# Kernel optimization log

Measured on AMD Instinct MI355X. Metric: run time of the kernel, lower is better.

## Reference

```python
import jax, jax.numpy as jnp
import numpy as np

N_NODES = 500_000
N_EDGES = 32_000_000
D_COEF = 1.0  # 'd' init arg, constant


def setup_inputs() -> dict:
    key = jax.random.key(0)
    k1, k2, k3 = jax.random.split(key, 3)
    theta = jax.random.normal(k1, (N_NODES, 1), dtype=jnp.float32)
    src = jax.random.randint(k2, (N_EDGES,), 0, N_NODES, dtype=jnp.int32)
    dst = jax.random.randint(k3, (N_EDGES,), 0, N_NODES, dtype=jnp.int32)
    logc = jnp.asarray(np.log(1.5), dtype=jnp.float32)  # continuousTimeVicsek2D.logc
    u0 = jnp.asarray(0.3, dtype=jnp.float32)
    return {"theta": theta, "logc": logc, "u0": u0, "src": src, "dst": dst}


def reference(theta, logc, u0, src, dst):
    # calc_message: dtheta = theta[src] - theta[dst]; m = exp(logc)*sin(d*dtheta)
    dtheta = theta[src] - theta[dst]              # [E,1] edge gather
    msg = jnp.exp(logc) * jnp.sin(dtheta * D_COEF)  # [E,1]
    # aggregate_message: mean over each node's incoming mailbox (segment mean by dst)
    n = theta.shape[0]
    w_sum = jax.ops.segment_sum(msg, dst, num_segments=n)          # [N,1]
    cnt = jax.ops.segment_sum(jnp.ones((dst.shape[0], 1), msg.dtype), dst, num_segments=n)
    w = w_sum / jnp.maximum(cnt, 1.0)             # [N,1] torque (0 if no in-edges)
    # polarity2velocity: v = u0 * [cos(theta), sin(theta)]
    v = u0 * jnp.concatenate([jnp.cos(theta), jnp.sin(theta)], axis=-1)  # [N,2]
    # return torque and velocity concatenated: [N,3] = [w | v]
    return jnp.concatenate([w, v], axis=-1)
```

## Files before the change

kernel.cpp:

```cpp
#include <hip/hip_runtime.h>


#define NB 123
#define BSHIFT 12
#define NODES_PER_B 4096
#define CAPB 272000u
#define TPB 256
#define EPT 16
#define EPI (TPB * EPT)
#define K_SLICES 8
#define TPB_R 512
#define Q_MASK 0xFFFFFu
#define DL_SHIFT 20

typedef int iv4 __attribute__((ext_vector_type(4)));

__device__ __forceinline__ float theta_l2(const float* p) {
    return __hip_atomic_load(p, __ATOMIC_RELAXED, __HIP_MEMORY_SCOPE_AGENT);
}

__global__ __launch_bounds__(TPB) void scatter_kernel(
    const float* __restrict__ theta,
    const int* __restrict__ src,
    const int* __restrict__ dst,
    unsigned int* __restrict__ recs,
    unsigned int* __restrict__ cursors,
    int n_edges, int n_iters)
{
    __shared__ unsigned int hist[NB];
    __shared__ unsigned int rankc[NB];
    __shared__ unsigned int offs[NB];
    __shared__ unsigned int gbase[NB];
    __shared__ unsigned int wsum0;
    __shared__ unsigned int sbuf[EPI];
    __shared__ unsigned char sbkt[EPI];

    const int tid = threadIdx.x;

    for (int iter = blockIdx.x; iter < n_iters; iter += gridDim.x) {
        const int base = iter * EPI + tid * EPT;

        for (int j = tid; j < NB; j += TPB) { hist[j] = 0; rankc[j] = 0; }
        __syncthreads();

        unsigned int myrec[EPT];
        int myb[EPT];

        if (base + EPT <= n_edges) {
            iv4 s4[4], d4[4];
            #pragma unroll
            for (int q = 0; q < 4; ++q) {
                s4[q] = __builtin_nontemporal_load(((const iv4*)(src + base)) + q);
                d4[q] = __builtin_nontemporal_load(((const iv4*)(dst + base)) + q);
            }
            const int* sp = (const int*)s4;
            const int* dp = (const int*)d4;
            float tg[EPT];
            #pragma unroll
            for (int j = 0; j < EPT; ++j) tg[j] = theta_l2(theta + sp[j]);
            #pragma unroll
            for (int j = 0; j < EPT; ++j) {
                int b = dp[j] >> BSHIFT;
                myb[j] = b;
                atomicAdd(&hist[b], 1u);
            }
            #pragma unroll
            for (int j = 0; j < EPT; ++j) {
                float tc = fminf(fmaxf(tg[j], -8.0f), 8.0f);
                unsigned int q = (unsigned int)fmaf(tc, 65536.0f, 524288.5f);
                if (q > Q_MASK) q = Q_MASK;
                myrec[j] = (((unsigned int)(dp[j] & (NODES_PER_B - 1))) << DL_SHIFT) | q;
            }
        } else {
            #pragma unroll
            for (int j = 0; j < EPT; ++j) {
                int e = base + j;
                if (e < n_edges) {
                    int dn = dst[e];
                    float tc = fminf(fmaxf(theta_l2(theta + src[e]), -8.0f), 8.0f);
                    unsigned int q = (unsigned int)fmaf(tc, 65536.0f, 524288.5f);
                    if (q > Q_MASK) q = Q_MASK;
                    myrec[j] = (((unsigned int)(dn & (NODES_PER_B - 1))) << DL_SHIFT) | q;
                    int b = dn >> BSHIFT;
                    myb[j] = b;
                    atomicAdd(&hist[b], 1u);
                } else {
                    myb[j] = -1;
                }
            }
        }
        __syncthreads();

        unsigned int h = 0, x = 0;
        if (tid < 128) {
            h = (tid < NB) ? hist[tid] : 0u;
            x = h;
            #pragma unroll
            for (int dlt = 1; dlt < 64; dlt <<= 1) {
                unsigned int y = __shfl_up(x, dlt, 64);
                if ((tid & 63) >= dlt) x += y;
            }
            if (tid == 63) wsum0 = x;
        }
        __syncthreads();
        if (tid < 128) {
            if (tid >= 64) x += wsum0;
            if (tid < NB) {
                offs[tid] = x - h;
                gbase[tid] = h ? atomicAdd(&cursors[tid], h) : 0u;
            }
        }
        __syncthreads();

        #pragma unroll
        for (int j = 0; j < EPT; ++j) {
            int b = myb[j];
            if (b >= 0) {
                unsigned int r = atomicAdd(&rankc[b], 1u);
                unsigned int slot = offs[b] + r;
                sbuf[slot] = myrec[j];
                sbkt[slot] = (unsigned char)b;
            }
        }
        __syncthreads();

        unsigned int total = offs[NB - 1] + hist[NB - 1];
        for (unsigned int slot = tid; slot < total; slot += TPB) {
            unsigned int b = sbkt[slot];
            unsigned int gpos = gbase[b] + (slot - offs[b]);
            if (gpos < CAPB) recs[(size_t)b * CAPB + gpos] = sbuf[slot];
        }
        __syncthreads();
    }
}

__device__ __forceinline__ void proc_rec(unsigned int ru, unsigned long long* acc)
{
    float t = fmaf((float)(ru & Q_MASK), 1.0f / 65536.0f, -8.0f);
    float s, co;
    __sincosf(t, &s, &co);
    unsigned int ps = (unsigned int)fmaf(s, 8192.0f, 16384.5f);
    unsigned int pc = (unsigned int)fmaf(co, 8192.0f, 16384.5f);
    atomicAdd(&acc[ru >> DL_SHIFT],
              ((unsigned long long)ps << 37) | ((unsigned long long)pc << 10) | 1ull);
}

__global__ __launch_bounds__(TPB_R, 8) void reduce_kernel(
    const unsigned int* __restrict__ recs,
    const unsigned int* __restrict__ cursors,
    unsigned long long* __restrict__ acc_g)
{
    __shared__ unsigned long long acc[NODES_PER_B];
    const int tid = threadIdx.x;
    const int b = blockIdx.x >> 3;
    const int k = blockIdx.x & 7;

    for (int j = tid; j < NODES_PER_B; j += TPB_R) acc[j] = 0ull;
    __syncthreads();

    unsigned int cnt = cursors[b];
    if (cnt > CAPB) cnt = CAPB;
    unsigned int slice = (((cnt + K_SLICES - 1) / K_SLICES) + 15u) & ~15u;
    unsigned int lo = (unsigned int)k * slice;
    if (lo > cnt) lo = cnt;
    unsigned int hi = lo + slice; if (hi > cnt) hi = cnt;

    const unsigned int* bp = recs + (size_t)b * CAPB;

    const unsigned int chunk = TPB_R * 4u;
    unsigned int nfull = (hi > lo) ? (hi - lo) / chunk : 0u;
    unsigned int vend = lo + nfull * chunk;

    for (unsigned int b2 = lo; b2 < vend; b2 += chunk) {
        uint4 r = *(const uint4*)(bp + b2 + (unsigned int)tid * 4u);
        proc_rec(r.x, acc);
        proc_rec(r.y, acc);
        proc_rec(r.z, acc);
        proc_rec(r.w, acc);
    }
    for (unsigned int j = vend + tid; j < hi; j += TPB_R) proc_rec(bp[j], acc);
    __syncthreads();

    unsigned long long* ag = acc_g + (size_t)b * NODES_PER_B;
    for (int j = tid; j < NODES_PER_B; j += TPB_R) {
        unsigned long long v = acc[j];
        if (v) atomicAdd(&ag[j], v);
    }
}

__global__ __launch_bounds__(TPB) void node_kernel(
    const float* __restrict__ theta,
    const float* __restrict__ logc,
    const float* __restrict__ u0p,
    const unsigned long long* __restrict__ acc_g,
    float* __restrict__ out,
    int n_nodes)
{
    int i = blockIdx.x * TPB + threadIdx.x;
    if (i >= n_nodes) return;

    unsigned long long a = acc_g[i];
    int cnt = (int)(a & 1023ull);
    int pcS = (int)((a >> 10) & 0x7FFFFFFull);
    int psS = (int)(a >> 37);
    float sinS = (float)(psS - cnt * 16384) * (1.0f / 8192.0f);
    float cosS = (float)(pcS - cnt * 16384) * (1.0f / 8192.0f);

    float t = theta[i];
    float sd, cd;
    __sincosf(t, &sd, &cd);
    float c = __expf(logc[0]);
    float w = c * (cd * sinS - sd * cosS) / fmaxf((float)cnt, 1.0f);
    float u0 = u0p[0];
    out[3 * i + 0] = w;
    out[3 * i + 1] = u0 * cd;
    out[3 * i + 2] = u0 * sd;
}

__global__ __launch_bounds__(256) void edge_kernel_fb(
    const float* __restrict__ theta, const float* __restrict__ logc,
    const int* __restrict__ src, const int* __restrict__ dst,
    unsigned long long* __restrict__ acc, int n_edges)
{
    const float c = __expf(logc[0]);
    int base = (blockIdx.x * 256 + threadIdx.x) * 4;
    if (base + 3 < n_edges) {
        int4 s4 = *(const int4*)(src + base);
        int4 d4 = *(const int4*)(dst + base);
        float m0 = c * __sinf(theta[s4.x] - theta[d4.x]);
        float m1 = c * __sinf(theta[s4.y] - theta[d4.y]);
        float m2 = c * __sinf(theta[s4.z] - theta[d4.z]);
        float m3 = c * __sinf(theta[s4.w] - theta[d4.w]);
        atomicAdd(&acc[d4.x], ((unsigned long long)((m0 + 2.0f) * 1073741824.0f) << 24) | 1ull);
        atomicAdd(&acc[d4.y], ((unsigned long long)((m1 + 2.0f) * 1073741824.0f) << 24) | 1ull);
        atomicAdd(&acc[d4.z], ((unsigned long long)((m2 + 2.0f) * 1073741824.0f) << 24) | 1ull);
        atomicAdd(&acc[d4.w], ((unsigned long long)((m3 + 2.0f) * 1073741824.0f) << 24) | 1ull);
    } else {
        for (int e = base; e < n_edges; ++e) {
            int s = src[e], d = dst[e];
            float m = c * __sinf(theta[s] - theta[d]);
            atomicAdd(&acc[d], ((unsigned long long)((m + 2.0f) * 1073741824.0f) << 24) | 1ull);
        }
    }
}

__global__ __launch_bounds__(256) void node_kernel_fb(
    const float* __restrict__ theta, const float* __restrict__ u0p,
    const unsigned long long* __restrict__ acc, float* __restrict__ out, int n_nodes)
{
    int i = blockIdx.x * 256 + threadIdx.x;
    if (i >= n_nodes) return;
    unsigned long long p = acc[i];
    long long cnt = (long long)(p & 0xFFFFFFull);
    long long net = (long long)(p >> 24) - (cnt << 31);
    float sum = (float)((double)net * (1.0 / 1073741824.0));
    float w = sum / fmaxf((float)cnt, 1.0f);
    float t = theta[i]; float u0 = u0p[0];
    out[3 * i + 0] = w;
    out[3 * i + 1] = u0 * __cosf(t);
    out[3 * i + 2] = u0 * __sinf(t);
}

extern "C" void kernel_launch(void* const* d_in, const int* in_sizes, int n_in,
                              void* d_out, int out_size, void* d_ws, size_t ws_size,
                              hipStream_t stream) {
    const float* theta = (const float*)d_in[0];
    const float* logc  = (const float*)d_in[1];
    const float* u0    = (const float*)d_in[2];
    const int*   src   = (const int*)d_in[3];
    const int*   dst   = (const int*)d_in[4];
    float* out = (float*)d_out;

    int n_nodes = in_sizes[0];
    int n_edges = in_sizes[3];

    size_t recs_bytes  = (size_t)NB * CAPB * sizeof(unsigned int);
    size_t cursors_off = (recs_bytes + 255) & ~(size_t)255;
    size_t acc_off     = cursors_off + 512;
    size_t acc_bytes   = (size_t)NB * NODES_PER_B * sizeof(unsigned long long);
    size_t need = acc_off + acc_bytes;

    bool fast = (ws_size >= need) && (n_nodes <= NB * NODES_PER_B);

    if (fast) {
        unsigned int* recs          = (unsigned int*)d_ws;
        unsigned int* cursors       = (unsigned int*)((char*)d_ws + cursors_off);
        unsigned long long* acc_g   = (unsigned long long*)((char*)d_ws + acc_off);

        (void)hipMemsetAsync(cursors, 0, 512 + acc_bytes, stream);

        int n_iters = (n_edges + EPI - 1) / EPI;
        scatter_kernel<<<n_iters, TPB, 0, stream>>>(theta, src, dst, recs,
                                                    cursors, n_edges, n_iters);

        reduce_kernel<<<NB * K_SLICES, TPB_R, 0, stream>>>(recs, cursors, acc_g);

        int nblocks = (n_nodes + TPB - 1) / TPB;
        node_kernel<<<nblocks, TPB, 0, stream>>>(theta, logc, u0, acc_g, out, n_nodes);
    } else {
        unsigned long long* acc = (unsigned long long*)d_ws;
        (void)hipMemsetAsync(d_ws, 0, (size_t)n_nodes * sizeof(unsigned long long), stream);
        int eblocks = (n_edges + 1023) / 1024;
        edge_kernel_fb<<<eblocks, 256, 0, stream>>>(theta, logc, src, dst, acc, n_edges);
        int nblocks = (n_nodes + 255) / 256;
        node_kernel_fb<<<nblocks, 256, 0, stream>>>(theta, u0, acc, out, n_nodes);
    }
}
```

Before: 482.1 us.

## Replace bucketed scatter/reduce with direct global 64-bit packed atomics per edge

Drops the two-pass bucket scatter into a record workspace followed by per-bucket LDS reduction. Each edge now computes sin/cos of its source theta and adds a packed 64-bit value straight into a global per-node accumulator. This removes the record write and re-read and the LDS bucketing passes, but sends 32M random 64-bit atomics to global memory/L2. It also removes the fallback path and the workspace-size check.

```diff
diff --git a/kernel.cpp b/kernel.cpp
--- a/kernel.cpp
+++ b/kernel.cpp
@@ -1,190 +1,55 @@
 #include <hip/hip_runtime.h>
 
 
-#define NB 123
-#define BSHIFT 12
-#define NODES_PER_B 4096
-#define CAPB 272000u
 #define TPB 256
 #define EPT 16
 #define EPI (TPB * EPT)
-#define K_SLICES 8
-#define TPB_R 512
-#define Q_MASK 0xFFFFFu
-#define DL_SHIFT 20
 
 typedef int iv4 __attribute__((ext_vector_type(4)));
 
-__device__ __forceinline__ float theta_l2(const float* p) {
-    return __hip_atomic_load(p, __ATOMIC_RELAXED, __HIP_MEMORY_SCOPE_AGENT);
-}
-
-__global__ __launch_bounds__(TPB) void scatter_kernel(
+__global__ __launch_bounds__(TPB) void edge_lin_kernel(
     const float* __restrict__ theta,
     const int* __restrict__ src,
     const int* __restrict__ dst,
-    unsigned int* __restrict__ recs,
-    unsigned int* __restrict__ cursors,
-    int n_edges, int n_iters)
+    unsigned long long* __restrict__ acc,
+    int n_edges)
 {
-    __shared__ unsigned int hist[NB];
-    __shared__ unsigned int rankc[NB];
-    __shared__ unsigned int offs[NB];
-    __shared__ unsigned int gbase[NB];
-    __shared__ unsigned int wsum0;
-    __shared__ unsigned int sbuf[EPI];
-    __shared__ unsigned char sbkt[EPI];
+    const int base = (blockIdx.x * TPB + threadIdx.x) * EPT;
 
-    const int tid = threadIdx.x;
+    if (base + EPT <= n_edges) {
+        iv4 s4[4], d4[4];
+        #pragma unroll
+        for (int q = 0; q < 4; ++q) {
+            s4[q] = __builtin_nontemporal_load(((const iv4*)(src + base)) + q);
+            d4[q] = __builtin_nontemporal_load(((const iv4*)(dst + base)) + q);
+        }
+        const int* sp = (const int*)s4;
+        const int* dp = (const int*)d4;
 
-    for (int iter = blockIdx.x; iter < n_iters; iter += gridDim.x) {
-        const int base = iter * EPI + tid * EPT;
-
-        for (int j = tid; j < NB; j += TPB) { hist[j] = 0; rankc[j] = 0; }
-        __syncthreads();
-
-        unsigned int myrec[EPT];
-        int myb[EPT];
-
-        if (base + EPT <= n_edges) {
-            iv4 s4[4], d4[4];
-            #pragma unroll
-            for (int q = 0; q < 4; ++q) {
-                s4[q] = __builtin_nontemporal_load(((const iv4*)(src + base)) + q);
-                d4[q] = __builtin_nontemporal_load(((const iv4*)(dst + base)) + q);
-            }
-            const int* sp = (const int*)s4;
-            const int* dp = (const int*)d4;
-            float tg[EPT];
-            #pragma unroll
-            for (int j = 0; j < EPT; ++j) tg[j] = theta_l2(theta + sp[j]);
-            #pragma unroll
-            for (int j = 0; j < EPT; ++j) {
-                int b = dp[j] >> BSHIFT;
-                myb[j] = b;
-                atomicAdd(&hist[b], 1u);
-            }
-            #pragma unroll
-            for (int j = 0; j < EPT; ++j) {
-                float tc = fminf(fmaxf(tg[j], -8.0f), 8.0f);
-                unsigned int q = (unsigned int)fmaf(tc, 65536.0f, 524288.5f);
-                if (q > Q_MASK) q = Q_MASK;
-                myrec[j] = (((unsigned int)(dp[j] & (NODES_PER_B - 1))) << DL_SHIFT) | q;
-            }
-        } else {
-            #pragma unroll
-            for (int j = 0; j < EPT; ++j) {
-                int e = base + j;
-                if (e < n_edges) {
-                    int dn = dst[e];
-                    float tc = fminf(fmaxf(theta_l2(theta + src[e]), -8.0f), 8.0f);
-                    unsigned int q = (unsigned int)fmaf(tc, 65536.0f, 524288.5f);
-                    if (q > Q_MASK) q = Q_MASK;
-                    myrec[j] = (((unsigned int)(dn & (NODES_PER_B - 1))) << DL_SHIFT) | q;
-                    int b = dn >> BSHIFT;
-                    myb[j] = b;
-                    atomicAdd(&hist[b], 1u);
-                } else {
-                    myb[j] = -1;
-                }
-            }
-        }
-        __syncthreads();
-
-        unsigned int h = 0, x = 0;
-        if (tid < 128) {
-            h = (tid < NB) ? hist[tid] : 0u;
-            x = h;
-            #pragma unroll
-            for (int dlt = 1; dlt < 64; dlt <<= 1) {
-                unsigned int y = __shfl_up(x, dlt, 64);
-                if ((tid & 63) >= dlt) x += y;
-            }
-            if (tid == 63) wsum0 = x;
-        }
-        __syncthreads();
-        if (tid < 128) {
-            if (tid >= 64) x += wsum0;
-            if (tid < NB) {
-                offs[tid] = x - h;
-                gbase[tid] = h ? atomicAdd(&cursors[tid], h) : 0u;
-            }
-        }
-        __syncthreads();
+        float tg[EPT];
+        #pragma unroll
+        for (int j = 0; j < EPT; ++j) tg[j] = theta[sp[j]];
 
         #pragma unroll
         for (int j = 0; j < EPT; ++j) {
-            int b = myb[j];
-            if (b >= 0) {
-                unsigned int r = atomicAdd(&rankc[b], 1u);
-                unsigned int slot = offs[b] + r;
-                sbuf[slot] = myrec[j];
-                sbkt[slot] = (unsigned char)b;
-            }
+            float s, co;
+            __sincosf(tg[j], &s, &co);
+            unsigned int ps = (unsigned int)fmaf(s,  8192.0f, 16384.5f);
+            unsigned int pc = (unsigned int)fmaf(co, 8192.0f, 16384.5f);
+            atomicAdd(&acc[dp[j]],
+                      ((unsigned long long)ps << 37) |
+                      ((unsigned long long)pc << 10) | 1ull);
         }
-        __syncthreads();
-
-        unsigned int total = offs[NB - 1] + hist[NB - 1];
-        for (unsigned int slot = tid; slot < total; slot += TPB) {
-            unsigned int b = sbkt[slot];
-            unsigned int gpos = gbase[b] + (slot - offs[b]);
-            if (gpos < CAPB) recs[(size_t)b * CAPB + gpos] = sbuf[slot];
+    } else {
+        for (int e = base; e < n_edges; ++e) {
+            float s, co;
+            __sincosf(theta[src[e]], &s, &co);
+            unsigned int ps = (unsigned int)fmaf(s,  8192.0f, 16384.5f);
+            unsigned int pc = (unsigned int)fmaf(co, 8192.0f, 16384.5f);
+            atomicAdd(&acc[dst[e]],
+                      ((unsigned long long)ps << 37) |
+                      ((unsigned long long)pc << 10) | 1ull);
         }
-        __syncthreads();
-    }
-}
-
-__device__ __forceinline__ void proc_rec(unsigned int ru, unsigned long long* acc)
-{
-    float t = fmaf((float)(ru & Q_MASK), 1.0f / 65536.0f, -8.0f);
-    float s, co;
-    __sincosf(t, &s, &co);
-    unsigned int ps = (unsigned int)fmaf(s, 8192.0f, 16384.5f);
-    unsigned int pc = (unsigned int)fmaf(co, 8192.0f, 16384.5f);
-    atomicAdd(&acc[ru >> DL_SHIFT],
-              ((unsigned long long)ps << 37) | ((unsigned long long)pc << 10) | 1ull);
-}
-
-__global__ __launch_bounds__(TPB_R, 8) void reduce_kernel(
-    const unsigned int* __restrict__ recs,
-    const unsigned int* __restrict__ cursors,
-    unsigned long long* __restrict__ acc_g)
-{
-    __shared__ unsigned long long acc[NODES_PER_B];
-    const int tid = threadIdx.x;
-    const int b = blockIdx.x >> 3;
-    const int k = blockIdx.x & 7;
-
-    for (int j = tid; j < NODES_PER_B; j += TPB_R) acc[j] = 0ull;
-    __syncthreads();
-
-    unsigned int cnt = cursors[b];
-    if (cnt > CAPB) cnt = CAPB;
-    unsigned int slice = (((cnt + K_SLICES - 1) / K_SLICES) + 15u) & ~15u;
-    unsigned int lo = (unsigned int)k * slice;
-    if (lo > cnt) lo = cnt;
-    unsigned int hi = lo + slice; if (hi > cnt) hi = cnt;
-
-    const unsigned int* bp = recs + (size_t)b * CAPB;
-
-    const unsigned int chunk = TPB_R * 4u;
-    unsigned int nfull = (hi > lo) ? (hi - lo) / chunk : 0u;
-    unsigned int vend = lo + nfull * chunk;
-
-    for (unsigned int b2 = lo; b2 < vend; b2 += chunk) {
-        uint4 r = *(const uint4*)(bp + b2 + (unsigned int)tid * 4u);
-        proc_rec(r.x, acc);
-        proc_rec(r.y, acc);
-        proc_rec(r.z, acc);
-        proc_rec(r.w, acc);
-    }
-    for (unsigned int j = vend + tid; j < hi; j += TPB_R) proc_rec(bp[j], acc);
-    __syncthreads();
-
-    unsigned long long* ag = acc_g + (size_t)b * NODES_PER_B;
-    for (int j = tid; j < NODES_PER_B; j += TPB_R) {
-        unsigned long long v = acc[j];
-        if (v) atomicAdd(&ag[j], v);
     }
 }
 
@@ -192,14 +57,14 @@
     const float* __restrict__ theta,
     const float* __restrict__ logc,
     const float* __restrict__ u0p,
-    const unsigned long long* __restrict__ acc_g,
+    const unsigned long long* __restrict__ acc,
     float* __restrict__ out,
     int n_nodes)
 {
     int i = blockIdx.x * TPB + threadIdx.x;
     if (i >= n_nodes) return;
 
-    unsigned long long a = acc_g[i];
+    unsigned long long a = acc[i];
     int cnt = (int)(a & 1023ull);
     int pcS = (int)((a >> 10) & 0x7FFFFFFull);
     int psS = (int)(a >> 37);
@@ -220,45 +85,9 @@
 __global__ __launch_bounds__(256) void edge_kernel_fb(
     const float* __restrict__ theta, const float* __restrict__ logc,
     const int* __restrict__ src, const int* __restrict__ dst,
-    unsigned long long* __restrict__ acc, int n_edges)
+    float* __restrict__ out, int n_edges)
 {
-    const float c = __expf(logc[0]);
-    int base = (blockIdx.x * 256 + threadIdx.x) * 4;
-    if (base + 3 < n_edges) {
-        int4 s4 = *(const int4*)(src + base);
-        int4 d4 = *(const int4*)(dst + base);
-        float m0 = c * __sinf(theta[s4.x] - theta[d4.x]);
-        float m1 = c * __sinf(theta[s4.y] - theta[d4.y]);
-        float m2 = c * __sinf(theta[s4.z] - theta[d4.z]);
-        float m3 = c * __sinf(theta[s4.w] - theta[d4.w]);
-        atomicAdd(&acc[d4.x], ((unsigned long long)((m0 + 2.0f) * 1073741824.0f) << 24) | 1ull);
-        atomicAdd(&acc[d4.y], ((unsigned long long)((m1 + 2.0f) * 1073741824.0f) << 24) | 1ull);
-        atomicAdd(&acc[d4.z], ((unsigned long long)((m2 + 2.0f) * 1073741824.0f) << 24) | 1ull);
-        atomicAdd(&acc[d4.w], ((unsigned long long)((m3 + 2.0f) * 1073741824.0f) << 24) | 1ull);
-    } else {
-        for (int e = base; e < n_edges; ++e) {
-            int s = src[e], d = dst[e];
-            float m = c * __sinf(theta[s] - theta[d]);
-            atomicAdd(&acc[d], ((unsigned long long)((m + 2.0f) * 1073741824.0f) << 24) | 1ull);
-        }
-    }
-}
-
-__global__ __launch_bounds__(256) void node_kernel_fb(
-    const float* __restrict__ theta, const float* __restrict__ u0p,
-    const unsigned long long* __restrict__ acc, float* __restrict__ out, int n_nodes)
-{
-    int i = blockIdx.x * 256 + threadIdx.x;
-    if (i >= n_nodes) return;
-    unsigned long long p = acc[i];
-    long long cnt = (long long)(p & 0xFFFFFFull);
-    long long net = (long long)(p >> 24) - (cnt << 31);
-    float sum = (float)((double)net * (1.0 / 1073741824.0));
-    float w = sum / fmaxf((float)cnt, 1.0f);
-    float t = theta[i]; float u0 = u0p[0];
-    out[3 * i + 0] = w;
-    out[3 * i + 1] = u0 * __cosf(t);
-    out[3 * i + 2] = u0 * __sinf(t);
+    (void)theta; (void)logc; (void)src; (void)dst; (void)out; (void)n_edges;
 }
 
 extern "C" void kernel_launch(void* const* d_in, const int* in_sizes, int n_in,
@@ -274,35 +103,14 @@
     int n_nodes = in_sizes[0];
     int n_edges = in_sizes[3];
 
-    size_t recs_bytes  = (size_t)NB * CAPB * sizeof(unsigned int);
-    size_t cursors_off = (recs_bytes + 255) & ~(size_t)255;
-    size_t acc_off     = cursors_off + 512;
-    size_t acc_bytes   = (size_t)NB * NODES_PER_B * sizeof(unsigned long long);
-    size_t need = acc_off + acc_bytes;
+    unsigned long long* acc = (unsigned long long*)d_ws;
 
-    bool fast = (ws_size >= need) && (n_nodes <= NB * NODES_PER_B);
+    (void)hipMemsetAsync(acc, 0, (size_t)n_nodes * sizeof(unsigned long long),
+                         stream);
 
-    if (fast) {
-        unsigned int* recs          = (unsigned int*)d_ws;
-        unsigned int* cursors       = (unsigned int*)((char*)d_ws + cursors_off);
-        unsigned long long* acc_g   = (unsigned long long*)((char*)d_ws + acc_off);
+    int eblocks = (n_edges + EPI - 1) / EPI;
+    edge_lin_kernel<<<eblocks, TPB, 0, stream>>>(theta, src, dst, acc, n_edges);
 
-        (void)hipMemsetAsync(cursors, 0, 512 + acc_bytes, stream);
-
-        int n_iters = (n_edges + EPI - 1) / EPI;
-        scatter_kernel<<<n_iters, TPB, 0, stream>>>(theta, src, dst, recs,
-                                                    cursors, n_edges, n_iters);
-
-        reduce_kernel<<<NB * K_SLICES, TPB_R, 0, stream>>>(recs, cursors, acc_g);
-
-        int nblocks = (n_nodes + TPB - 1) / TPB;
-        node_kernel<<<nblocks, TPB, 0, stream>>>(theta, logc, u0, acc_g, out, n_nodes);
-    } else {
-        unsigned long long* acc = (unsigned long long*)d_ws;
-        (void)hipMemsetAsync(d_ws, 0, (size_t)n_nodes * sizeof(unsigned long long), stream);
-        int eblocks = (n_edges + 1023) / 1024;
-        edge_kernel_fb<<<eblocks, 256, 0, stream>>>(theta, logc, src, dst, acc, n_edges);
-        int nblocks = (n_nodes + 255) / 256;
-        node_kernel_fb<<<nblocks, 256, 0, stream>>>(theta, u0, acc, out, n_nodes);
-    }
+    int nblocks = (n_nodes + TPB - 1) / TPB;
+    node_kernel<<<nblocks, TPB, 0, stream>>>(theta, logc, u0, acc, out, n_nodes);
 }
```

Result: slower. 1.589 ms (+229.6%).

## Write per-slice partials instead of global atomics, reuse histogram ranks, nontemporal stores

Applied to the files above, without the earlier changes.

The reduce kernel now writes each slice's shared-memory accumulator into its own partials buffer instead of atomically adding into a global accumulator. The node kernel sums the 8 slices per node, which removes the large memset and the global atomics. The scatter kernel takes each edge's rank from the histogram atomic's return value, dropping the second rank-counter atomic pass. Theta gathers become plain loads, and record stores and loads become nontemporal. The cost is more partials memory (8x) and 8 reads per node in the final kernel.

```diff
diff --git a/kernel.cpp b/kernel.cpp
--- a/kernel.cpp
+++ b/kernel.cpp
@@ -14,10 +14,7 @@
 #define DL_SHIFT 20
 
 typedef int iv4 __attribute__((ext_vector_type(4)));
-
-__device__ __forceinline__ float theta_l2(const float* p) {
-    return __hip_atomic_load(p, __ATOMIC_RELAXED, __HIP_MEMORY_SCOPE_AGENT);
-}
+typedef unsigned int uv4 __attribute__((ext_vector_type(4)));
 
 __global__ __launch_bounds__(TPB) void scatter_kernel(
     const float* __restrict__ theta,
@@ -28,7 +25,6 @@
     int n_edges, int n_iters)
 {
     __shared__ unsigned int hist[NB];
-    __shared__ unsigned int rankc[NB];
     __shared__ unsigned int offs[NB];
     __shared__ unsigned int gbase[NB];
     __shared__ unsigned int wsum0;
@@ -40,11 +36,11 @@
     for (int iter = blockIdx.x; iter < n_iters; iter += gridDim.x) {
         const int base = iter * EPI + tid * EPT;
 
-        for (int j = tid; j < NB; j += TPB) { hist[j] = 0; rankc[j] = 0; }
+        for (int j = tid; j < NB; j += TPB) hist[j] = 0;
         __syncthreads();
 
         unsigned int myrec[EPT];
-        int myb[EPT];
+        unsigned int mybr[EPT];
 
         if (base + EPT <= n_edges) {
             iv4 s4[4], d4[4];
@@ -57,12 +53,12 @@
             const int* dp = (const int*)d4;
             float tg[EPT];
             #pragma unroll
-            for (int j = 0; j < EPT; ++j) tg[j] = theta_l2(theta + sp[j]);
+            for (int j = 0; j < EPT; ++j) tg[j] = theta[sp[j]];
             #pragma unroll
             for (int j = 0; j < EPT; ++j) {
                 int b = dp[j] >> BSHIFT;
-                myb[j] = b;
-                atomicAdd(&hist[b], 1u);
+                unsigned int r = atomicAdd(&hist[b], 1u);
+                mybr[j] = ((unsigned int)b << 12) | r;
             }
             #pragma unroll
             for (int j = 0; j < EPT; ++j) {
@@ -77,15 +73,15 @@
                 int e = base + j;
                 if (e < n_edges) {
                     int dn = dst[e];
-                    float tc = fminf(fmaxf(theta_l2(theta + src[e]), -8.0f), 8.0f);
+                    float tc = fminf(fmaxf(theta[src[e]], -8.0f), 8.0f);
                     unsigned int q = (unsigned int)fmaf(tc, 65536.0f, 524288.5f);
                     if (q > Q_MASK) q = Q_MASK;
                     myrec[j] = (((unsigned int)(dn & (NODES_PER_B - 1))) << DL_SHIFT) | q;
                     int b = dn >> BSHIFT;
-                    myb[j] = b;
-                    atomicAdd(&hist[b], 1u);
+                    unsigned int r = atomicAdd(&hist[b], 1u);
+                    mybr[j] = ((unsigned int)b << 12) | r;
                 } else {
-                    myb[j] = -1;
+                    mybr[j] = 0xFFFFFFFFu;
                 }
             }
         }
@@ -114,10 +110,10 @@
 
         #pragma unroll
         for (int j = 0; j < EPT; ++j) {
-            int b = myb[j];
-            if (b >= 0) {
-                unsigned int r = atomicAdd(&rankc[b], 1u);
-                unsigned int slot = offs[b] + r;
+            unsigned int br = mybr[j];
+            if (br != 0xFFFFFFFFu) {
+                unsigned int b = br >> 12;
+                unsigned int slot = offs[b] + (br & 4095u);
                 sbuf[slot] = myrec[j];
                 sbkt[slot] = (unsigned char)b;
             }
@@ -128,7 +124,9 @@
         for (unsigned int slot = tid; slot < total; slot += TPB) {
             unsigned int b = sbkt[slot];
             unsigned int gpos = gbase[b] + (slot - offs[b]);
-            if (gpos < CAPB) recs[(size_t)b * CAPB + gpos] = sbuf[slot];
+            if (gpos < CAPB)
+                __builtin_nontemporal_store(sbuf[slot],
+                                            recs + (size_t)b * CAPB + gpos);
         }
         __syncthreads();
     }
@@ -148,7 +146,7 @@
 __global__ __launch_bounds__(TPB_R, 8) void reduce_kernel(
     const unsigned int* __restrict__ recs,
     const unsigned int* __restrict__ cursors,
-    unsigned long long* __restrict__ acc_g)
+    unsigned long long* __restrict__ partials)
 {
     __shared__ unsigned long long acc[NODES_PER_B];
     const int tid = threadIdx.x;
@@ -172,7 +170,8 @@
     unsigned int vend = lo + nfull * chunk;
 
     for (unsigned int b2 = lo; b2 < vend; b2 += chunk) {
-        uint4 r = *(const uint4*)(bp + b2 + (unsigned int)tid * 4u);
+        uv4 r = __builtin_nontemporal_load(
+            (const uv4*)(bp + b2 + (unsigned int)tid * 4u));
         proc_rec(r.x, acc);
         proc_rec(r.y, acc);
         proc_rec(r.z, acc);
@@ -181,28 +180,32 @@
     for (unsigned int j = vend + tid; j < hi; j += TPB_R) proc_rec(bp[j], acc);
     __syncthreads();
 
-    unsigned long long* ag = acc_g + (size_t)b * NODES_PER_B;
-    for (int j = tid; j < NODES_PER_B; j += TPB_R) {
-        unsigned long long v = acc[j];
-        if (v) atomicAdd(&ag[j], v);
-    }
+    unsigned long long* pb = partials + (size_t)blockIdx.x * NODES_PER_B;
+    for (int j = tid; j < NODES_PER_B; j += TPB_R) pb[j] = acc[j];
 }
 
 __global__ __launch_bounds__(TPB) void node_kernel(
     const float* __restrict__ theta,
     const float* __restrict__ logc,
     const float* __restrict__ u0p,
-    const unsigned long long* __restrict__ acc_g,
+    const unsigned long long* __restrict__ partials,
     float* __restrict__ out,
     int n_nodes)
 {
     int i = blockIdx.x * TPB + threadIdx.x;
     if (i >= n_nodes) return;
-
-    unsigned long long a = acc_g[i];
-    int cnt = (int)(a & 1023ull);
-    int pcS = (int)((a >> 10) & 0x7FFFFFFull);
-    int psS = (int)(a >> 37);
+    int b = i >> BSHIFT;
+    int l = i & (NODES_PER_B - 1);
+
+    int cnt = 0, psS = 0, pcS = 0;
+    #pragma unroll
+    for (int k = 0; k < K_SLICES; ++k) {
+        unsigned long long a =
+            partials[(size_t)(b * K_SLICES + k) * NODES_PER_B + l];
+        cnt += (int)(a & 1023ull);
+        pcS += (int)((a >> 10) & 0x7FFFFFFull);
+        psS += (int)(a >> 37);
+    }
     float sinS = (float)(psS - cnt * 16384) * (1.0f / 8192.0f);
     float cosS = (float)(pcS - cnt * 16384) * (1.0f / 8192.0f);
 
@@ -274,35 +277,43 @@
     int n_nodes = in_sizes[0];
     int n_edges = in_sizes[3];
 
-    size_t recs_bytes  = (size_t)NB * CAPB * sizeof(unsigned int);
-    size_t cursors_off = (recs_bytes + 255) & ~(size_t)255;
-    size_t acc_off     = cursors_off + 512;
-    size_t acc_bytes   = (size_t)NB * NODES_PER_B * sizeof(unsigned long long);
-    size_t need = acc_off + acc_bytes;
+    size_t recs_bytes     = (size_t)NB * CAPB * sizeof(unsigned int);
+    size_t cursors_off    = (recs_bytes + 255) & ~(size_t)255;
+    size_t partials_off   = (cursors_off + 512 + 255) & ~(size_t)255;
+    size_t partials_bytes = (size_t)NB * K_SLICES * NODES_PER_B
+                          * sizeof(unsigned long long);
+    size_t need = partials_off + partials_bytes;
 
     bool fast = (ws_size >= need) && (n_nodes <= NB * NODES_PER_B);
 
     if (fast) {
-        unsigned int* recs          = (unsigned int*)d_ws;
-        unsigned int* cursors       = (unsigned int*)((char*)d_ws + cursors_off);
-        unsigned long long* acc_g   = (unsigned long long*)((char*)d_ws + acc_off);
-
-        (void)hipMemsetAsync(cursors, 0, 512 + acc_bytes, stream);
+        unsigned int* recs     = (unsigned int*)d_ws;
+        unsigned int* cursors  = (unsigned int*)((char*)d_ws + cursors_off);
+        unsigned long long* partials =
+            (unsigned long long*)((char*)d_ws + partials_off);
+
+        (void)hipMemsetAsync(cursors, 0, 512, stream);
 
         int n_iters = (n_edges + EPI - 1) / EPI;
         scatter_kernel<<<n_iters, TPB, 0, stream>>>(theta, src, dst, recs,
                                                     cursors, n_edges, n_iters);
 
-        reduce_kernel<<<NB * K_SLICES, TPB_R, 0, stream>>>(recs, cursors, acc_g);
+        reduce_kernel<<<NB * K_SLICES, TPB_R, 0, stream>>>(recs, cursors,
+                                                           partials);
 
         int nblocks = (n_nodes + TPB - 1) / TPB;
-        node_kernel<<<nblocks, TPB, 0, stream>>>(theta, logc, u0, acc_g, out, n_nodes);
+        node_kernel<<<nblocks, TPB, 0, stream>>>(theta, logc, u0, partials,
+                                                 out, n_nodes);
     } else {
         unsigned long long* acc = (unsigned long long*)d_ws;
-        (void)hipMemsetAsync(d_ws, 0, (size_t)n_nodes * sizeof(unsigned long long), stream);
+        (void)hipMemsetAsync(d_ws, 0,
+                             (size_t)n_nodes * sizeof(unsigned long long),
+                             stream);
         int eblocks = (n_edges + 1023) / 1024;
-        edge_kernel_fb<<<eblocks, 256, 0, stream>>>(theta, logc, src, dst, acc, n_edges);
+        edge_kernel_fb<<<eblocks, 256, 0, stream>>>(theta, logc, src, dst,
+                                                    acc, n_edges);
         int nblocks = (n_nodes + 255) / 256;
-        node_kernel_fb<<<nblocks, 256, 0, stream>>>(theta, u0, acc, out, n_nodes);
-    }
-}
+        node_kernel_fb<<<nblocks, 256, 0, stream>>>(theta, u0, acc, out,
+                                                    n_nodes);
+    }
+}
```

Measured after the change: 476.5 us. No clear change (-1.2%).

## Prefetch next edge tile in persistent scatter and gather 16-bit quantized theta

Applied to the files above, without the earlier changes.

A prep kernel now quantizes theta to 16-bit codes, which halves the footprint of the random gather table. The scatter kernel becomes a persistent loop over a capped grid that loads the next tile's src/dst and theta codes while the current tile is being binned. The histogram and rank pass are merged into a single LDS atomic that returns the rank, which drops the separate rankc array and one atomic per edge. Reduce loads become nontemporal. The risks are coarser theta quantization (16 bits instead of 20), higher register pressure from the double-buffered state, and one extra kernel launch.

```diff
diff --git a/kernel.cpp b/kernel.cpp
--- a/kernel.cpp
+++ b/kernel.cpp
@@ -12,15 +12,26 @@
 #define TPB_R 512
 #define Q_MASK 0xFFFFFu
 #define DL_SHIFT 20
+#define G_SCAT 1024
 
 typedef int iv4 __attribute__((ext_vector_type(4)));
-
-__device__ __forceinline__ float theta_l2(const float* p) {
-    return __hip_atomic_load(p, __ATOMIC_RELAXED, __HIP_MEMORY_SCOPE_AGENT);
+typedef unsigned int uv4 __attribute__((ext_vector_type(4)));
+
+__global__ __launch_bounds__(256) void prep_kernel(
+    const float* __restrict__ theta,
+    unsigned short* __restrict__ th16,
+    int n_nodes)
+{
+    int i = blockIdx.x * 256 + threadIdx.x;
+    if (i >= n_nodes) return;
+    float tc = fminf(fmaxf(theta[i], -8.0f), 8.0f);
+    unsigned int q = (unsigned int)fmaf(tc, 4096.0f, 32768.5f);
+    if (q > 65535u) q = 65535u;
+    th16[i] = (unsigned short)q;
 }
 
 __global__ __launch_bounds__(TPB) void scatter_kernel(
-    const float* __restrict__ theta,
+    const unsigned short* __restrict__ th16,
     const int* __restrict__ src,
     const int* __restrict__ dst,
     unsigned int* __restrict__ recs,
@@ -28,7 +39,6 @@
     int n_edges, int n_iters)
 {
     __shared__ unsigned int hist[NB];
-    __shared__ unsigned int rankc[NB];
     __shared__ unsigned int offs[NB];
     __shared__ unsigned int gbase[NB];
     __shared__ unsigned int wsum0;
@@ -36,16 +46,14 @@
     __shared__ unsigned char sbkt[EPI];
 
     const int tid = threadIdx.x;
-
-    for (int iter = blockIdx.x; iter < n_iters; iter += gridDim.x) {
+    int iter = blockIdx.x;
+    if (iter >= n_iters) return;
+
+    int sp[EPT], dp[EPT];
+    unsigned int tg[EPT];
+
+    {
         const int base = iter * EPI + tid * EPT;
-
-        for (int j = tid; j < NB; j += TPB) { hist[j] = 0; rankc[j] = 0; }
-        __syncthreads();
-
-        unsigned int myrec[EPT];
-        int myb[EPT];
-
         if (base + EPT <= n_edges) {
             iv4 s4[4], d4[4];
             #pragma unroll
@@ -53,40 +61,65 @@
                 s4[q] = __builtin_nontemporal_load(((const iv4*)(src + base)) + q);
                 d4[q] = __builtin_nontemporal_load(((const iv4*)(dst + base)) + q);
             }
-            const int* sp = (const int*)s4;
-            const int* dp = (const int*)d4;
-            float tg[EPT];
-            #pragma unroll
-            for (int j = 0; j < EPT; ++j) tg[j] = theta_l2(theta + sp[j]);
             #pragma unroll
             for (int j = 0; j < EPT; ++j) {
-                int b = dp[j] >> BSHIFT;
-                myb[j] = b;
-                atomicAdd(&hist[b], 1u);
-            }
-            #pragma unroll
-            for (int j = 0; j < EPT; ++j) {
-                float tc = fminf(fmaxf(tg[j], -8.0f), 8.0f);
-                unsigned int q = (unsigned int)fmaf(tc, 65536.0f, 524288.5f);
-                if (q > Q_MASK) q = Q_MASK;
-                myrec[j] = (((unsigned int)(dp[j] & (NODES_PER_B - 1))) << DL_SHIFT) | q;
+                sp[j] = ((const int*)s4)[j];
+                dp[j] = ((const int*)d4)[j];
             }
         } else {
             #pragma unroll
             for (int j = 0; j < EPT; ++j) {
                 int e = base + j;
-                if (e < n_edges) {
-                    int dn = dst[e];
-                    float tc = fminf(fmaxf(theta_l2(theta + src[e]), -8.0f), 8.0f);
-                    unsigned int q = (unsigned int)fmaf(tc, 65536.0f, 524288.5f);
-                    if (q > Q_MASK) q = Q_MASK;
-                    myrec[j] = (((unsigned int)(dn & (NODES_PER_B - 1))) << DL_SHIFT) | q;
-                    int b = dn >> BSHIFT;
-                    myb[j] = b;
-                    atomicAdd(&hist[b], 1u);
-                } else {
-                    myb[j] = -1;
+                if (e < n_edges) { sp[j] = src[e]; dp[j] = dst[e]; }
+                else             { sp[j] = 0;      dp[j] = -1;     }
+            }
+        }
+        #pragma unroll
+        for (int j = 0; j < EPT; ++j) tg[j] = th16[sp[j]];
+    }
+
+    while (true) {
+        const int next = iter + gridDim.x;
+        const bool have_next = (next < n_iters);
+
+        int spn[EPT], dpn[EPT];
+        if (have_next) {
+            const int base2 = next * EPI + tid * EPT;
+            if (base2 + EPT <= n_edges) {
+                iv4 s4[4], d4[4];
+                #pragma unroll
+                for (int q = 0; q < 4; ++q) {
+                    s4[q] = __builtin_nontemporal_load(((const iv4*)(src + base2)) + q);
+                    d4[q] = __builtin_nontemporal_load(((const iv4*)(dst + base2)) + q);
                 }
+                #pragma unroll
+                for (int j = 0; j < EPT; ++j) {
+                    spn[j] = ((const int*)s4)[j];
+                    dpn[j] = ((const int*)d4)[j];
+                }
+            } else {
+                #pragma unroll
+                for (int j = 0; j < EPT; ++j) {
+                    int e = base2 + j;
+                    if (e < n_edges) { spn[j] = src[e]; dpn[j] = dst[e]; }
+                    else             { spn[j] = 0;      dpn[j] = -1;     }
+                }
+            }
+        }
+
+        for (int j = tid; j < NB; j += TPB) hist[j] = 0;
+        __syncthreads();
+
+        unsigned int mybr[EPT];
+        #pragma unroll
+        for (int j = 0; j < EPT; ++j) {
+            int dn = dp[j];
+            if (dn >= 0) {
+                int b = dn >> BSHIFT;
+                unsigned int r = atomicAdd(&hist[b], 1u);
+                mybr[j] = ((unsigned int)b << 12) | r;
+            } else {
+                mybr[j] = 0xFFFFFFFFu;
             }
         }
         __syncthreads();
@@ -114,13 +147,20 @@
 
         #pragma unroll
         for (int j = 0; j < EPT; ++j) {
-            int b = myb[j];
-            if (b >= 0) {
-                unsigned int r = atomicAdd(&rankc[b], 1u);
-                unsigned int slot = offs[b] + r;
-                sbuf[slot] = myrec[j];
+            unsigned int br = mybr[j];
+            if (br != 0xFFFFFFFFu) {
+                unsigned int b = br >> 12;
+                unsigned int slot = offs[b] + (br & 4095u);
+                sbuf[slot] = (((unsigned int)(dp[j] & (NODES_PER_B - 1))) << DL_SHIFT)
+                           | (tg[j] << 4);
                 sbkt[slot] = (unsigned char)b;
             }
+        }
+
+        unsigned int tgn[EPT];
+        if (have_next) {
+            #pragma unroll
+            for (int j = 0; j < EPT; ++j) tgn[j] = th16[spn[j]];
         }
         __syncthreads();
 
@@ -130,7 +170,15 @@
             unsigned int gpos = gbase[b] + (slot - offs[b]);
             if (gpos < CAPB) recs[(size_t)b * CAPB + gpos] = sbuf[slot];
         }
-        __syncthreads();
+
+        if (!have_next) break;
+        __syncthreads();
+
+        iter = next;
+        #pragma unroll
+        for (int j = 0; j < EPT; ++j) {
+            sp[j] = spn[j]; dp[j] = dpn[j]; tg[j] = tgn[j];
+        }
     }
 }
 
@@ -172,7 +220,8 @@
     unsigned int vend = lo + nfull * chunk;
 
     for (unsigned int b2 = lo; b2 < vend; b2 += chunk) {
-        uint4 r = *(const uint4*)(bp + b2 + (unsigned int)tid * 4u);
+        uv4 r = __builtin_nontemporal_load(
+            (const uv4*)(bp + b2 + (unsigned int)tid * 4u));
         proc_rec(r.x, acc);
         proc_rec(r.y, acc);
         proc_rec(r.z, acc);
@@ -278,31 +327,43 @@
     size_t cursors_off = (recs_bytes + 255) & ~(size_t)255;
     size_t acc_off     = cursors_off + 512;
     size_t acc_bytes   = (size_t)NB * NODES_PER_B * sizeof(unsigned long long);
-    size_t need = acc_off + acc_bytes;
+    size_t th16_off    = (acc_off + acc_bytes + 255) & ~(size_t)255;
+    size_t th16_bytes  = (size_t)NB * NODES_PER_B * sizeof(unsigned short);
+    size_t need = th16_off + th16_bytes;
 
     bool fast = (ws_size >= need) && (n_nodes <= NB * NODES_PER_B);
 
     if (fast) {
-        unsigned int* recs          = (unsigned int*)d_ws;
-        unsigned int* cursors       = (unsigned int*)((char*)d_ws + cursors_off);
-        unsigned long long* acc_g   = (unsigned long long*)((char*)d_ws + acc_off);
+        unsigned int* recs        = (unsigned int*)d_ws;
+        unsigned int* cursors     = (unsigned int*)((char*)d_ws + cursors_off);
+        unsigned long long* acc_g = (unsigned long long*)((char*)d_ws + acc_off);
+        unsigned short* th16      = (unsigned short*)((char*)d_ws + th16_off);
 
         (void)hipMemsetAsync(cursors, 0, 512 + acc_bytes, stream);
 
+        int pblocks = (n_nodes + 255) / 256;
+        prep_kernel<<<pblocks, 256, 0, stream>>>(theta, th16, n_nodes);
+
         int n_iters = (n_edges + EPI - 1) / EPI;
-        scatter_kernel<<<n_iters, TPB, 0, stream>>>(theta, src, dst, recs,
-                                                    cursors, n_edges, n_iters);
+        int g = n_iters < G_SCAT ? n_iters : G_SCAT;
+        scatter_kernel<<<g, TPB, 0, stream>>>(th16, src, dst, recs, cursors,
+                                              n_edges, n_iters);
 
         reduce_kernel<<<NB * K_SLICES, TPB_R, 0, stream>>>(recs, cursors, acc_g);
 
         int nblocks = (n_nodes + TPB - 1) / TPB;
-        node_kernel<<<nblocks, TPB, 0, stream>>>(theta, logc, u0, acc_g, out, n_nodes);
+        node_kernel<<<nblocks, TPB, 0, stream>>>(theta, logc, u0, acc_g, out,
+                                                 n_nodes);
     } else {
         unsigned long long* acc = (unsigned long long*)d_ws;
-        (void)hipMemsetAsync(d_ws, 0, (size_t)n_nodes * sizeof(unsigned long long), stream);
+        (void)hipMemsetAsync(d_ws, 0,
+                             (size_t)n_nodes * sizeof(unsigned long long),
+                             stream);
         int eblocks = (n_edges + 1023) / 1024;
-        edge_kernel_fb<<<eblocks, 256, 0, stream>>>(theta, logc, src, dst, acc, n_edges);
+        edge_kernel_fb<<<eblocks, 256, 0, stream>>>(theta, logc, src, dst,
+                                                    acc, n_edges);
         int nblocks = (n_nodes + 255) / 256;
-        node_kernel_fb<<<nblocks, 256, 0, stream>>>(theta, u0, acc, out, n_nodes);
-    }
-}
+        node_kernel_fb<<<nblocks, 256, 0, stream>>>(theta, u0, acc, out,
+                                                    n_nodes);
+    }
+}
```

Measured after the change: 468.8 us. 1.03x faster.
